# Optimization experiments

Hardware: AMD Instinct MI355X
Metric: run time of the kernel (lower is better)

The kernel has to match this reference:

```python
import jax, jax.numpy as jnp
import numpy as np

B, C, H, W = 8, 64, 256, 256
S = 512          # style_dim
K = 3            # modulated conv kernel
LRELU_SLOPE = 0.2
FUSED_SCALE = float(np.sqrt(2.0))
LIN_SCALE = 1.0 / float(np.sqrt(S))          # EqualLinear scale
CONV_SCALE = 1.0 / float(np.sqrt(C * K * K)) # ModulatedConv2d scale


def setup_inputs() -> dict:
    key = jax.random.key(0)
    ks = jax.random.split(key, 8)
    kaiming = float(np.sqrt(2.0 / (C * 9)))  # torch Conv2d default-ish init scale
    return {
        "x": jax.random.normal(ks[0], (B, C, H, W), jnp.float32),
        "style": jax.random.normal(ks[1], (B, S), jnp.float32),
        # bottleneck_IR block 1 (bn=False -> Identity norms, shortcut=identity)
        "w1a": jax.random.normal(ks[2], (C, C, 3, 3), jnp.float32) * kaiming,
        "alpha1": jnp.full((C,), 0.25, jnp.float32),
        "w1b": jax.random.normal(ks[3], (C, C, 3, 3), jnp.float32) * kaiming,
        # bottleneck_IR block 2
        "w2a": jax.random.normal(ks[4], (C, C, 3, 3), jnp.float32) * kaiming,
        "alpha2": jnp.full((C,), 0.25, jnp.float32),
        "w2b": jax.random.normal(ks[5], (C, C, 3, 3), jnp.float32) * kaiming,
        # ModulatedConv2d: EqualLinear(S->C, bias_init=1) + weight [out,in,k,k]
        "mod_w": jax.random.normal(ks[6], (C, S), jnp.float32),
        "mod_b": jnp.ones((C,), jnp.float32),
        "conv_w": jax.random.normal(ks[7], (C, C, K, K), jnp.float32),
        # FusedLeakyReLU bias
        "fused_b": jnp.zeros((C,), jnp.float32),
    }


def _conv3(x, w):
    return jax.lax.conv_general_dilated(
        x, w, (1, 1), "SAME", dimension_numbers=("NCHW", "OIHW", "NCHW"))


def _prelu(x, a):
    return jnp.where(x > 0, x, a[None, :, None, None] * x)


def _bottleneck_ir(x, wa, alpha, wb):
    # shortcut is identity (in_channel==depth, stride=1); norms are Identity (bn=False)
    return x + _conv3(_prelu(_conv3(x, wa), alpha), wb)


def reference(x, style, w1a, alpha1, w1b, w2a, alpha2, w2b,
              mod_w, mod_b, conv_w, fused_b):
    h = _bottleneck_ir(x, w1a, alpha1, w1b)
    h = _bottleneck_ir(h, w2a, alpha2, w2b)

    # ModulatedConv2d (stride 1, no up/down sample, demodulate=True)
    s = style @ (mod_w.T * LIN_SCALE) + mod_b              # [B, Cin]
    w = CONV_SCALE * conv_w[None] * s[:, None, :, None, None]  # [B, Cout, Cin, K, K]
    demod = jax.lax.rsqrt(jnp.sum(w * w, axis=(2, 3, 4)) + 1e-8)
    w = w * demod[:, :, None, None, None]

    Bn, Cin, Hh, Ww = h.shape
    out = jax.lax.conv_general_dilated(
        h.reshape(1, Bn * Cin, Hh, Ww),            # grouped-conv trick
        w.reshape(Bn * C, Cin, K, K),
        (1, 1), "SAME",
        dimension_numbers=("NCHW", "OIHW", "NCHW"),
        feature_group_count=Bn,
    ).reshape(Bn, C, Hh, Ww)

    # FusedLeakyReLU: (x + bias) -> leaky_relu(0.2) -> * sqrt(2)
    ob = out + fused_b[None, :, None, None]
    return jnp.where(ob > 0, ob, LRELU_SLOPE * ob) * FUSED_SCALE
```

## Files before the change

### kernel.cpp

```cpp
#include <hip/hip_runtime.h>
#include <hip/hip_bf16.h>
#include <math.h>

#define BB 8
#define SS 512
#define LIN_SCALE 0.044194173824159216f
#define CONV_SCALE 0.041666666666666664f
#define SQRT2 1.4142135623730951f

typedef __attribute__((ext_vector_type(8))) short short8;
typedef __attribute__((ext_vector_type(16))) float f32x16;

__device__ __forceinline__ ushort bf16h(float v) {
    unsigned u = __float_as_uint(v);
    return (ushort)((u + 0x7fffu + ((u >> 16) & 1u)) >> 16);
}
__device__ __forceinline__ void splitv(float v, ushort& h, ushort& l) {
    h = bf16h(v);
    l = bf16h(v - __uint_as_float((unsigned)h << 16));
}
__device__ __forceinline__ float b2f(ushort u) { return __uint_as_float((unsigned)u << 16); }


__global__ void zero_k(float* z) { z[threadIdx.x] = 0.f; }

__global__ __launch_bounds__(256) void tocl_k(const float* __restrict__ x,
                                              ushort* __restrict__ oCL) {
    __shared__ float tile[64][65];
    const int blk = blockIdx.x;
    const int b = blk >> 10, rem = blk & 1023;
    const int y = rem >> 2, x0 = (rem & 3) << 6;
    const int tid = threadIdx.x, lane = tid & 63, g = tid >> 6;
    const float* xb = x + ((size_t)b << 22) + (y << 8) + x0;
    #pragma unroll
    for (int i = 0; i < 16; ++i) {
        int c = i * 4 + g;
        tile[c][lane] = xb[((size_t)c << 16) + lane];
    }
    __syncthreads();
    const int cc = tid >> 6, xx = tid & 63;
    ushort hh[16], ll[16];
    #pragma unroll
    for (int t = 0; t < 16; ++t) splitv(tile[cc * 16 + t][xx], hh[t], ll[t]);
    uint w[16];
    #pragma unroll
    for (int i = 0; i < 8; ++i) {
        w[i]     = (uint)hh[2 * i] | ((uint)hh[2 * i + 1] << 16);
        w[8 + i] = (uint)ll[2 * i] | ((uint)ll[2 * i + 1] << 16);
    }
    ushort* dst = oCL + ((((size_t)(b * 4 + cc)) << 16) + (y << 8) + x0 + xx) * 32;
    *(uint4*)(dst +  0) = make_uint4(w[0], w[1], w[2], w[3]);
    *(uint4*)(dst +  8) = make_uint4(w[4], w[5], w[6], w[7]);
    *(uint4*)(dst + 16) = make_uint4(w[8], w[9], w[10], w[11]);
    *(uint4*)(dst + 24) = make_uint4(w[12], w[13], w[14], w[15]);
}

__device__ __forceinline__ int wsrc_idx(int i, int& pl) {
    int e = i & 7;
    int j = (i % 18432) >> 3;
    int cc = i / 18432;
    int F = j >> 6, u = j & 63;
    int ln_ = u >> 1, lh_ = u & 1;
    int m = F & 1; pl = (F >> 1) & 1;
    int td = F >> 2;
    int dx = td / 3, dy = td - 3 * dx;
    int co = m * 32 + ln_;
    int ci = cc * 16 + lh_ * 8 + e;
    return (co * 64 + ci) * 9 + dy * 3 + dx;
}

__global__ void packw_k(const float* __restrict__ w, ushort* __restrict__ img) {
    int i = blockIdx.x * 256 + threadIdx.x;
    if (i >= 73728) return;
    int pl; int src = wsrc_idx(i, pl);
    ushort h, l; splitv(w[src], h, l);
    img[i] = pl ? l : h;
}

__global__ void style_s_k(const float* __restrict__ style, const float* __restrict__ mod_w,
                          const float* __restrict__ mod_b, float* __restrict__ sbuf) {
    int tid = threadIdx.x;
    int b = tid >> 6, cin = tid & 63;
    float acc = 0.f;
    for (int j = 0; j < SS; ++j) acc += style[b * SS + j] * mod_w[cin * SS + j];
    sbuf[b * 64 + cin] = acc * LIN_SCALE + mod_b[cin];
}

__global__ void demod_k(const float* __restrict__ conv_w, const float* __restrict__ sbuf,
                        float* __restrict__ demod) {
    int tid = threadIdx.x;
    int b = tid >> 6, cout = tid & 63;
    float sum = 0.f;
    for (int cin = 0; cin < 64; ++cin) {
        float m = CONV_SCALE * sbuf[b * 64 + cin];
        const float* wp = conv_w + (cout * 64 + cin) * 9;
        #pragma unroll
        for (int k = 0; k < 9; ++k) { float v = wp[k] * m; sum += v * v; }
    }
    demod[b * 64 + cout] = 1.0f / sqrtf(sum + 1e-8f);
}

__global__ void packmod_k(const float* __restrict__ conv_w, const float* __restrict__ sbuf,
                          const float* __restrict__ demod, ushort* __restrict__ img) {
    int i = blockIdx.x * 256 + threadIdx.x;
    if (i >= 589824) return;
    int b = i / 73728, ii = i % 73728;
    int pl; int src = wsrc_idx(ii, pl);
    int co = src / 576; int ci = (src / 9) % 64;
    float v = CONV_SCALE * conv_w[src] * sbuf[b * 64 + ci] * demod[b * 64 + co];
    ushort h, l; splitv(v, h, l);
    img[i] = pl ? l : h;
}

#define GLDS(gsrc, ldst) __builtin_amdgcn_global_load_lds( \
    (const __attribute__((address_space(1))) unsigned int*)(gsrc), \
    (__attribute__((address_space(3))) unsigned int*)(ldst), 16, 0, 0)

#define VWAIT0 asm volatile("s_waitcnt vmcnt(0)" ::: "memory")
#define BAR    __builtin_amdgcn_s_barrier()
#define SCB    __builtin_amdgcn_sched_barrier(0)
#define MFMA32(a, bb, c) __builtin_amdgcn_mfma_f32_32x32x16_bf16(a, bb, c, 0, 0, 0)

template <int EPI, int PERB>
__global__ __launch_bounds__(256, 1)
void mconv_k(const ushort* __restrict__ inCL, const ushort* __restrict__ wimg,
             const float* __restrict__ aux, const ushort* __restrict__ rCL,
             ushort* __restrict__ oCL, float* __restrict__ onchw,
             const ushort* __restrict__ zb) {
    __shared__ __align__(16) char lds[155648];
    const int tid = threadIdx.x;
    const int orig = blockIdx.x;
    const int blk = (orig & 7) * 128 + (orig >> 3);
    const int b = blk >> 7, t7 = blk & 127;
    const int y0 = (t7 >> 3) << 4, x0 = (t7 & 7) << 5;
    const int wv = tid >> 6, l = tid & 63, ln = l & 31, lh = l >> 5;

    const ushort* wsrc = wimg + (PERB ? (size_t)b * 73728 : 0);

    f32x16 acc[2][4];
    #pragma unroll
    for (int m = 0; m < 2; ++m)
        #pragma unroll
        for (int j = 0; j < 4; ++j) acc[m][j] = (f32x16)(0.0f);

#define ISSUE_IN(cc, bo) { \
    _Pragma("unroll") for (int r_ = 0; r_ < 10; ++r_) { \
        const int s_ = r_ * 256 + tid; \
        const int p_ = s_ >> 2, sp_ = s_ & 3; \
        const int k_ = (sp_ - (p_ >> 1)) & 3; \
        const int row_ = p_ / 34, u_ = p_ - row_ * 34; \
        const int gy_ = y0 - 1 + row_, gx_ = x0 + u_ - 1; \
        const bool ok_ = ((unsigned)gy_ < 256u) & ((unsigned)gx_ < 256u) & (p_ < 612); \
        const ushort* src_ = ok_ \
            ? inCL + ((((size_t)(b * 4 + (cc))) << 16) + (gy_ << 8) + gx_) * 32 + k_ * 8 \
            : zb; \
        GLDS(src_, lds + (bo) + r_ * 4096 + (tid & 192) * 16); \
    } }

#define ISSUE_W(cc, bo) { \
    const ushort* wsB_ = wsrc + (cc) * 18432; \
    _Pragma("unroll") for (int r_ = 0; r_ < 9; ++r_) \
        GLDS(wsB_ + r_ * 2048 + tid * 8, lds + (bo) + r_ * 4096 + (tid & 192) * 16); }

#define PHASE(C, DX) { \
    const char* ib_ = lds + ((C) & 1) * 40960; \
    const char* wb_ = lds + 81920 + ((C) & 1) * 36864; \
    short8 bH_[6], bL_[6]; \
    _Pragma("unroll") for (int r_ = 0; r_ < 6; ++r_) { \
        const int p_ = (4 * wv + r_) * 34 + ln + (DX); \
        const int gH_ = 4 * p_ + ((lh + (p_ >> 1)) & 3); \
        const int gL_ = 4 * p_ + ((2 + lh + (p_ >> 1)) & 3); \
        bH_[r_] = *(const short8*)(ib_ + gH_ * 16); \
        bL_[r_] = *(const short8*)(ib_ + gL_ * 16); \
    } \
    _Pragma("unroll") for (int dy_ = 0; dy_ < 3; ++dy_) { \
        const char* wa_ = wb_ + ((DX) * 3 + dy_) * 4096 + (ln * 2 + lh) * 16; \
        const short8 aH0_ = *(const short8*)(wa_); \
        const short8 aH1_ = *(const short8*)(wa_ + 1024); \
        const short8 aL0_ = *(const short8*)(wa_ + 2048); \
        const short8 aL1_ = *(const short8*)(wa_ + 3072); \
        _Pragma("unroll") for (int j_ = 0; j_ < 4; ++j_) { \
            const int r_ = j_ + dy_; \
            acc[0][j_] = MFMA32(aH0_, bH_[r_], acc[0][j_]); \
            acc[0][j_] = MFMA32(aH0_, bL_[r_], acc[0][j_]); \
            acc[0][j_] = MFMA32(aL0_, bH_[r_], acc[0][j_]); \
            acc[1][j_] = MFMA32(aH1_, bH_[r_], acc[1][j_]); \
            acc[1][j_] = MFMA32(aH1_, bL_[r_], acc[1][j_]); \
            acc[1][j_] = MFMA32(aL1_, bH_[r_], acc[1][j_]); \
        } \
    } }

#define CHUNK(C) { \
    if ((C) < 3) { ISSUE_IN((C) + 1, (((C) + 1) & 1) * 40960); \
                   ISSUE_W((C) + 1, 81920 + (((C) + 1) & 1) * 36864); } \
    PHASE(C, 0); PHASE(C, 1); PHASE(C, 2); \
    if ((C) < 3) { SCB; VWAIT0; BAR; SCB; } }

    ISSUE_IN(0, 0);
    ISSUE_W(0, 81920);
    SCB; VWAIT0; BAR; SCB;

    CHUNK(0); CHUNK(1); CHUNK(2); CHUNK(3);

#undef ISSUE_IN
#undef ISSUE_W
#undef PHASE
#undef CHUNK

    #pragma unroll
    for (int m = 0; m < 2; ++m)
        #pragma unroll
        for (int j = 0; j < 4; ++j) {
            const int yo = y0 + 4 * wv + j;
            const int pixel = (yo << 8) + x0 + ln;
            #pragma unroll
            for (int q = 0; q < 4; ++q) {
                const int co0 = m * 32 + 8 * q + 4 * lh;
                float v0 = acc[m][j][4 * q + 0], v1 = acc[m][j][4 * q + 1];
                float v2 = acc[m][j][4 * q + 2], v3 = acc[m][j][4 * q + 3];
                const int cc_o = co0 >> 4, ch = co0 & 15;
                const size_t gbase = ((((size_t)(b * 4 + cc_o)) << 16) + pixel) * 32 + ch;
                if (EPI == 0) {
                    float4 al = *(const float4*)(aux + co0);
                    v0 = v0 > 0.f ? v0 : al.x * v0;
                    v1 = v1 > 0.f ? v1 : al.y * v1;
                    v2 = v2 > 0.f ? v2 : al.z * v2;
                    v3 = v3 > 0.f ? v3 : al.w * v3;
                } else if (EPI == 1) {
                    ushort4 rh = *(const ushort4*)(rCL + gbase);
                    ushort4 rl = *(const ushort4*)(rCL + gbase + 16);
                    v0 += b2f(rh.x) + b2f(rl.x);
                    v1 += b2f(rh.y) + b2f(rl.y);
                    v2 += b2f(rh.z) + b2f(rl.z);
                    v3 += b2f(rh.w) + b2f(rl.w);
                } else {
                    float4 bi = *(const float4*)(aux + co0);
                    float ob;
                    ob = v0 + bi.x; v0 = (ob > 0.f ? ob : 0.2f * ob) * SQRT2;
                    ob = v1 + bi.y; v1 = (ob > 0.f ? ob : 0.2f * ob) * SQRT2;
                    ob = v2 + bi.z; v2 = (ob > 0.f ? ob : 0.2f * ob) * SQRT2;
                    ob = v3 + bi.w; v3 = (ob > 0.f ? ob : 0.2f * ob) * SQRT2;
                }
                if (EPI == 2) {
                    const size_t sp = (size_t)pixel;
                    onchw[(((size_t)(b * 64 + co0 + 0)) << 16) + sp] = v0;
                    onchw[(((size_t)(b * 64 + co0 + 1)) << 16) + sp] = v1;
                    onchw[(((size_t)(b * 64 + co0 + 2)) << 16) + sp] = v2;
                    onchw[(((size_t)(b * 64 + co0 + 3)) << 16) + sp] = v3;
                } else {
                    ushort4 h4, l4;
                    splitv(v0, h4.x, l4.x); splitv(v1, h4.y, l4.y);
                    splitv(v2, h4.z, l4.z); splitv(v3, h4.w, l4.w);
                    *(ushort4*)(oCL + gbase) = h4;
                    *(ushort4*)(oCL + gbase + 16) = l4;
                }
            }
        }
}

extern "C" void kernel_launch(void* const* d_in, const int* in_sizes, int n_in,
                              void* d_out, int out_size, void* d_ws, size_t ws_size,
                              hipStream_t stream) {
    const float* x       = (const float*)d_in[0];
    const float* style   = (const float*)d_in[1];
    const float* w1a     = (const float*)d_in[2];
    const float* alpha1  = (const float*)d_in[3];
    const float* w1b     = (const float*)d_in[4];
    const float* w2a     = (const float*)d_in[5];
    const float* alpha2  = (const float*)d_in[6];
    const float* w2b     = (const float*)d_in[7];
    const float* mod_w   = (const float*)d_in[8];
    const float* mod_b   = (const float*)d_in[9];
    const float* conv_w  = (const float*)d_in[10];
    const float* fused_b = (const float*)d_in[11];
    float* out = (float*)d_out;

    char* ws = (char*)d_ws;
    float*  zbf   = (float*)ws;
    float*  sbuf  = (float*)(ws + 256);
    float*  demod = (float*)(ws + 2304);
    ushort* wfix  = (ushort*)(ws + 4352);
    ushort* wmod  = (ushort*)(ws + 594176);
    char*   pl    = ws + 1774080;
    const size_t PAIRB = 134217728ull;

    ushort* XP = (ushort*)pl;
    ushort* PB = (ushort*)(pl + PAIRB);
    ushort* PA;
    if (ws_size >= 1774080ull + 3 * PAIRB) PA = (ushort*)(pl + 2 * PAIRB);
    else                                   PA = (ushort*)d_out;
    const ushort* zb = (const ushort*)zbf;

    hipLaunchKernelGGL(zero_k, dim3(1), dim3(64), 0, stream, zbf);
    hipLaunchKernelGGL(tocl_k, dim3(BB * 1024), dim3(256), 0, stream, x, XP);
    hipLaunchKernelGGL(packw_k, dim3(288), dim3(256), 0, stream, w1a, wfix + 0 * 73728);
    hipLaunchKernelGGL(packw_k, dim3(288), dim3(256), 0, stream, w1b, wfix + 1 * 73728);
    hipLaunchKernelGGL(packw_k, dim3(288), dim3(256), 0, stream, w2a, wfix + 2 * 73728);
    hipLaunchKernelGGL(packw_k, dim3(288), dim3(256), 0, stream, w2b, wfix + 3 * 73728);
    hipLaunchKernelGGL(style_s_k, dim3(1), dim3(512), 0, stream, style, mod_w, mod_b, sbuf);
    hipLaunchKernelGGL(demod_k, dim3(1), dim3(512), 0, stream, conv_w, sbuf, demod);
    hipLaunchKernelGGL(packmod_k, dim3(2304), dim3(256), 0, stream, conv_w, sbuf, demod, wmod);

    const dim3 cgrid(1024), cblk(256);
    hipLaunchKernelGGL((mconv_k<0, 0>), cgrid, cblk, 0, stream,
        XP, wfix + 0 * 73728, alpha1, (const ushort*)nullptr, PA, (float*)nullptr, zb);
    hipLaunchKernelGGL((mconv_k<1, 0>), cgrid, cblk, 0, stream,
        PA, wfix + 1 * 73728, (const float*)nullptr, XP, PB, (float*)nullptr, zb);
    hipLaunchKernelGGL((mconv_k<0, 0>), cgrid, cblk, 0, stream,
        PB, wfix + 2 * 73728, alpha2, (const ushort*)nullptr, PA, (float*)nullptr, zb);
    hipLaunchKernelGGL((mconv_k<1, 0>), cgrid, cblk, 0, stream,
        PA, wfix + 3 * 73728, (const float*)nullptr, PB, PB, (float*)nullptr, zb);
    hipLaunchKernelGGL((mconv_k<2, 1>), cgrid, cblk, 0, stream,
        PB, wmod, fused_b, (const ushort*)nullptr, (ushort*)nullptr, out, zb);
}
```

Before: 964.0 us.

## Halve conv tile height, stream weights from global into registers, double occupancy

Changes the conv tile from 16x32 to 8x32 pixels, which doubles the grid, and cuts LDS to about 43KB so two blocks can share a CU (launch bounds set to 2). Weight fragments are no longer staged through LDS. Each lane now loads them from global memory into double-buffered registers, and the weight image layout is repacked so lane-contiguous reads work. It also adds s_setprio around the MFMA bursts and a partial vmcnt wait that lets in-flight register weight loads overlap the barrier. The cost is more redundant halo loads per output pixel, higher register pressure, and relying on global/L2 latency for the weight fetches.

```diff
diff --git a/kernel.cpp b/kernel.cpp
--- a/kernel.cpp
+++ b/kernel.cpp
@@ -55,25 +55,24 @@
     *(uint4*)(dst + 24) = make_uint4(w[12], w[13], w[14], w[15]);
 }
 
-__device__ __forceinline__ int wsrc_idx(int i, int& pl) {
-    int e = i & 7;
-    int j = (i % 18432) >> 3;
-    int cc = i / 18432;
-    int F = j >> 6, u = j & 63;
-    int ln_ = u >> 1, lh_ = u & 1;
-    int m = F & 1; pl = (F >> 1) & 1;
-    int td = F >> 2;
-    int dx = td / 3, dy = td - 3 * dx;
-    int co = m * 32 + ln_;
-    int ci = cc * 16 + lh_ * 8 + e;
-    return (co * 64 + ci) * 9 + dy * 3 + dx;
+__device__ __forceinline__ void wdecode(int i, int& c, int& tap, int& co, int& ci, int& pl) {
+    int e = i & 7;  int t = i >> 3;
+    int lh = t & 1; t >>= 1;
+    co = t & 63;    t >>= 6;
+    pl = t & 1;     t >>= 1;
+    int dy = t % 3; t /= 3;
+    int dx = t % 3; t /= 3;
+    c = t;
+    ci = c * 16 + lh * 8 + e;
+    tap = dy * 3 + dx;
 }
 
 __global__ void packw_k(const float* __restrict__ w, ushort* __restrict__ img) {
     int i = blockIdx.x * 256 + threadIdx.x;
     if (i >= 73728) return;
-    int pl; int src = wsrc_idx(i, pl);
-    ushort h, l; splitv(w[src], h, l);
+    int c, tap, co, ci, pl;
+    wdecode(i, c, tap, co, ci, pl);
+    ushort h, l; splitv(w[(co * 64 + ci) * 9 + tap], h, l);
     img[i] = pl ? l : h;
 }
 
@@ -105,9 +104,9 @@
     int i = blockIdx.x * 256 + threadIdx.x;
     if (i >= 589824) return;
     int b = i / 73728, ii = i % 73728;
-    int pl; int src = wsrc_idx(ii, pl);
-    int co = src / 576; int ci = (src / 9) % 64;
-    float v = CONV_SCALE * conv_w[src] * sbuf[b * 64 + ci] * demod[b * 64 + co];
+    int c, tap, co, ci, pl;
+    wdecode(ii, c, tap, co, ci, pl);
+    float v = CONV_SCALE * conv_w[(co * 64 + ci) * 9 + tap] * sbuf[b * 64 + ci] * demod[b * 64 + co];
     ushort h, l; splitv(v, h, l);
     img[i] = pl ? l : h;
 }
@@ -116,102 +115,121 @@
     (const __attribute__((address_space(1))) unsigned int*)(gsrc), \
     (__attribute__((address_space(3))) unsigned int*)(ldst), 16, 0, 0)
 
-#define VWAIT0 asm volatile("s_waitcnt vmcnt(0)" ::: "memory")
-#define BAR    __builtin_amdgcn_s_barrier()
-#define SCB    __builtin_amdgcn_sched_barrier(0)
+#define VWAIT12 asm volatile("s_waitcnt vmcnt(12)" ::: "memory")
+#define BAR     __builtin_amdgcn_s_barrier()
+#define SCB     __builtin_amdgcn_sched_barrier(0)
 #define MFMA32(a, bb, c) __builtin_amdgcn_mfma_f32_32x32x16_bf16(a, bb, c, 0, 0, 0)
 
 template <int EPI, int PERB>
-__global__ __launch_bounds__(256, 1)
+__global__ __launch_bounds__(256, 2)
 void mconv_k(const ushort* __restrict__ inCL, const ushort* __restrict__ wimg,
              const float* __restrict__ aux, const ushort* __restrict__ rCL,
              ushort* __restrict__ oCL, float* __restrict__ onchw,
              const ushort* __restrict__ zb) {
-    __shared__ __align__(16) char lds[155648];
+    __shared__ __align__(16) char lds[43520];
     const int tid = threadIdx.x;
     const int orig = blockIdx.x;
-    const int blk = (orig & 7) * 128 + (orig >> 3);
-    const int b = blk >> 7, t7 = blk & 127;
-    const int y0 = (t7 >> 3) << 4, x0 = (t7 & 7) << 5;
+    const int blk = (orig & 7) * 256 + (orig >> 3);
+    const int b = blk >> 8, t8 = blk & 255;
+    const int y0 = (t8 >> 3) << 3, x0 = (t8 & 7) << 5;
     const int wv = tid >> 6, l = tid & 63, ln = l & 31, lh = l >> 5;
 
     const ushort* wsrc = wimg + (PERB ? (size_t)b * 73728 : 0);
-
-    f32x16 acc[2][4];
+    const int aoff = ln * 16 + lh * 8;
+
+    f32x16 acc[2][2];
     #pragma unroll
     for (int m = 0; m < 2; ++m)
         #pragma unroll
-        for (int j = 0; j < 4; ++j) acc[m][j] = (f32x16)(0.0f);
+        for (int j = 0; j < 2; ++j) acc[m][j] = (f32x16)(0.0f);
+
+    short8 A0H[3][2], A0L[3][2], A1H[3][2], A1L[3][2];
 
 #define ISSUE_IN(cc, bo) { \
-    _Pragma("unroll") for (int r_ = 0; r_ < 10; ++r_) { \
-        const int s_ = r_ * 256 + tid; \
-        const int p_ = s_ >> 2, sp_ = s_ & 3; \
+    _Pragma("unroll") for (int r_ = 0; r_ < 5; ++r_) { \
+        const int G_ = r_ * 256 + tid; \
+        const int p_ = G_ >> 2, sp_ = G_ & 3; \
         const int k_ = (sp_ - (p_ >> 1)) & 3; \
         const int row_ = p_ / 34, u_ = p_ - row_ * 34; \
         const int gy_ = y0 - 1 + row_, gx_ = x0 + u_ - 1; \
-        const bool ok_ = ((unsigned)gy_ < 256u) & ((unsigned)gx_ < 256u) & (p_ < 612); \
+        const bool ok_ = ((unsigned)gy_ < 256u) & ((unsigned)gx_ < 256u); \
         const ushort* src_ = ok_ \
             ? inCL + ((((size_t)(b * 4 + (cc))) << 16) + (gy_ << 8) + gx_) * 32 + k_ * 8 \
             : zb; \
         GLDS(src_, lds + (bo) + r_ * 4096 + (tid & 192) * 16); \
+    } \
+    { const int G_ = 1280 + tid; \
+      const int p_ = G_ >> 2, sp_ = G_ & 3; \
+      const int k_ = (sp_ - (p_ >> 1)) & 3; \
+      const int row_ = p_ / 34, u_ = p_ - row_ * 34; \
+      const int gy_ = y0 - 1 + row_, gx_ = x0 + u_ - 1; \
+      const bool ok_ = (tid < 80) & ((unsigned)gy_ < 256u) & ((unsigned)gx_ < 256u); \
+      const ushort* src_ = ok_ \
+          ? inCL + ((((size_t)(b * 4 + (cc))) << 16) + (gy_ << 8) + gx_) * 32 + k_ * 8 \
+          : zb; \
+      if (tid < 80) GLDS(src_, lds + (bo) + 20480 + (tid & 192) * 16); } }
+
+#define LOADA(BNK, C, DX) { \
+    _Pragma("unroll") for (int dy_ = 0; dy_ < 3; ++dy_) { \
+        const ushort* ab_ = wsrc + (size_t)(((C) * 3 + (DX)) * 3 + dy_) * 2048 + aoff; \
+        BNK##H[dy_][0] = *(const short8*)ab_; \
+        BNK##H[dy_][1] = *(const short8*)(ab_ + 512); \
+        BNK##L[dy_][0] = *(const short8*)(ab_ + 1024); \
+        BNK##L[dy_][1] = *(const short8*)(ab_ + 1536); \
     } }
 
-#define ISSUE_W(cc, bo) { \
-    const ushort* wsB_ = wsrc + (cc) * 18432; \
-    _Pragma("unroll") for (int r_ = 0; r_ < 9; ++r_) \
-        GLDS(wsB_ + r_ * 2048 + tid * 8, lds + (bo) + r_ * 4096 + (tid & 192) * 16); }
-
-#define PHASE(C, DX) { \
-    const char* ib_ = lds + ((C) & 1) * 40960; \
-    const char* wb_ = lds + 81920 + ((C) & 1) * 36864; \
-    short8 bH_[6], bL_[6]; \
-    _Pragma("unroll") for (int r_ = 0; r_ < 6; ++r_) { \
-        const int p_ = (4 * wv + r_) * 34 + ln + (DX); \
+#define PHASE(C, DX, CUR) { \
+    const char* ib_ = lds + ((C) & 1) * 21760; \
+    short8 bH_[4], bL_[4]; \
+    _Pragma("unroll") for (int r_ = 0; r_ < 4; ++r_) { \
+        const int p_ = (2 * wv + r_) * 34 + ln + (DX); \
         const int gH_ = 4 * p_ + ((lh + (p_ >> 1)) & 3); \
         const int gL_ = 4 * p_ + ((2 + lh + (p_ >> 1)) & 3); \
         bH_[r_] = *(const short8*)(ib_ + gH_ * 16); \
         bL_[r_] = *(const short8*)(ib_ + gL_ * 16); \
     } \
-    _Pragma("unroll") for (int dy_ = 0; dy_ < 3; ++dy_) { \
-        const char* wa_ = wb_ + ((DX) * 3 + dy_) * 4096 + (ln * 2 + lh) * 16; \
-        const short8 aH0_ = *(const short8*)(wa_); \
-        const short8 aH1_ = *(const short8*)(wa_ + 1024); \
-        const short8 aL0_ = *(const short8*)(wa_ + 2048); \
-        const short8 aL1_ = *(const short8*)(wa_ + 3072); \
-        _Pragma("unroll") for (int j_ = 0; j_ < 4; ++j_) { \
+    __builtin_amdgcn_s_setprio(1); \
+    _Pragma("unroll") for (int dy_ = 0; dy_ < 3; ++dy_) \
+        _Pragma("unroll") for (int j_ = 0; j_ < 2; ++j_) { \
             const int r_ = j_ + dy_; \
-            acc[0][j_] = MFMA32(aH0_, bH_[r_], acc[0][j_]); \
-            acc[0][j_] = MFMA32(aH0_, bL_[r_], acc[0][j_]); \
-            acc[0][j_] = MFMA32(aL0_, bH_[r_], acc[0][j_]); \
-            acc[1][j_] = MFMA32(aH1_, bH_[r_], acc[1][j_]); \
-            acc[1][j_] = MFMA32(aH1_, bL_[r_], acc[1][j_]); \
-            acc[1][j_] = MFMA32(aL1_, bH_[r_], acc[1][j_]); \
+            acc[0][j_] = MFMA32(CUR##H[dy_][0], bH_[r_], acc[0][j_]); \
+            acc[0][j_] = MFMA32(CUR##H[dy_][0], bL_[r_], acc[0][j_]); \
+            acc[0][j_] = MFMA32(CUR##L[dy_][0], bH_[r_], acc[0][j_]); \
+            acc[1][j_] = MFMA32(CUR##H[dy_][1], bH_[r_], acc[1][j_]); \
+            acc[1][j_] = MFMA32(CUR##H[dy_][1], bL_[r_], acc[1][j_]); \
+            acc[1][j_] = MFMA32(CUR##L[dy_][1], bH_[r_], acc[1][j_]); \
         } \
-    } }
-
-#define CHUNK(C) { \
-    if ((C) < 3) { ISSUE_IN((C) + 1, (((C) + 1) & 1) * 40960); \
-                   ISSUE_W((C) + 1, 81920 + (((C) + 1) & 1) * 36864); } \
-    PHASE(C, 0); PHASE(C, 1); PHASE(C, 2); \
-    if ((C) < 3) { SCB; VWAIT0; BAR; SCB; } }
+    __builtin_amdgcn_s_setprio(0); }
 
     ISSUE_IN(0, 0);
-    ISSUE_W(0, 81920);
-    SCB; VWAIT0; BAR; SCB;
-
-    CHUNK(0); CHUNK(1); CHUNK(2); CHUNK(3);
+    LOADA(A0, 0, 0);
+    SCB; VWAIT12; BAR; SCB;
+
+    ISSUE_IN(1, 21760); LOADA(A1, 0, 1); PHASE(0, 0, A0);
+    LOADA(A0, 0, 2);                     PHASE(0, 1, A1);
+    LOADA(A1, 1, 0);                     PHASE(0, 2, A0);
+    SCB; VWAIT12; BAR; SCB;
+    ISSUE_IN(2, 0);     LOADA(A0, 1, 1); PHASE(1, 0, A1);
+    LOADA(A1, 1, 2);                     PHASE(1, 1, A0);
+    LOADA(A0, 2, 0);                     PHASE(1, 2, A1);
+    SCB; VWAIT12; BAR; SCB;
+    ISSUE_IN(3, 21760); LOADA(A1, 2, 1); PHASE(2, 0, A0);
+    LOADA(A0, 2, 2);                     PHASE(2, 1, A1);
+    LOADA(A1, 3, 0);                     PHASE(2, 2, A0);
+    SCB; VWAIT12; BAR; SCB;
+    LOADA(A0, 3, 1); PHASE(3, 0, A1);
+    LOADA(A1, 3, 2); PHASE(3, 1, A0);
+    PHASE(3, 2, A1);
 
 #undef ISSUE_IN
-#undef ISSUE_W
+#undef LOADA
 #undef PHASE
-#undef CHUNK
 
     #pragma unroll
     for (int m = 0; m < 2; ++m)
         #pragma unroll
-        for (int j = 0; j < 4; ++j) {
-            const int yo = y0 + 4 * wv + j;
+        for (int j = 0; j < 2; ++j) {
+            const int yo = y0 + 2 * wv + j;
             const int pixel = (yo << 8) + x0 + ln;
             #pragma unroll
             for (int q = 0; q < 4; ++q) {
@@ -301,7 +319,7 @@
     hipLaunchKernelGGL(demod_k, dim3(1), dim3(512), 0, stream, conv_w, sbuf, demod);
     hipLaunchKernelGGL(packmod_k, dim3(2304), dim3(256), 0, stream, conv_w, sbuf, demod, wmod);
 
-    const dim3 cgrid(1024), cblk(256);
+    const dim3 cgrid(2048), cblk(256);
     hipLaunchKernelGGL((mconv_k<0, 0>), cgrid, cblk, 0, stream,
         XP, wfix + 0 * 73728, alpha1, (const ushort*)nullptr, PA, (float*)nullptr, zb);
     hipLaunchKernelGGL((mconv_k<1, 0>), cgrid, cblk, 0, stream,
```

Result: no change. 951.0 us (-1.3%).

## Load input tiles directly to registers, shrink LDS for two blocks per CU

Applied to the files above, without the earlier changes.

Input activation tiles are no longer staged through LDS. Each lane now loads its high and low bf16 halves straight from global memory into registers, prefetching the next phase's high part while the current phase computes. LDS holds only the double-buffered weights, so it shrinks enough for launch bounds of two blocks per CU. MFMA sections are wrapped in raised wave priority, and the wait relaxes to vmcnt(6). The risks are redundant global loads across overlapping 3x3 halos, higher register pressure under the two-block bound, and a correctness dependence on the vmcnt counting matching the issued loads.

```diff
diff --git a/kernel.cpp b/kernel.cpp
--- a/kernel.cpp
+++ b/kernel.cpp
@@ -116,18 +116,18 @@
     (const __attribute__((address_space(1))) unsigned int*)(gsrc), \
     (__attribute__((address_space(3))) unsigned int*)(ldst), 16, 0, 0)
 
-#define VWAIT0 asm volatile("s_waitcnt vmcnt(0)" ::: "memory")
+#define VWAIT6 asm volatile("s_waitcnt vmcnt(6)" ::: "memory")
 #define BAR    __builtin_amdgcn_s_barrier()
 #define SCB    __builtin_amdgcn_sched_barrier(0)
 #define MFMA32(a, bb, c) __builtin_amdgcn_mfma_f32_32x32x16_bf16(a, bb, c, 0, 0, 0)
 
 template <int EPI, int PERB>
-__global__ __launch_bounds__(256, 1)
+__global__ __launch_bounds__(256, 2)
 void mconv_k(const ushort* __restrict__ inCL, const ushort* __restrict__ wimg,
              const float* __restrict__ aux, const ushort* __restrict__ rCL,
              ushort* __restrict__ oCL, float* __restrict__ onchw,
              const ushort* __restrict__ zb) {
-    __shared__ __align__(16) char lds[155648];
+    __shared__ __align__(16) char lds[73728];
     const int tid = threadIdx.x;
     const int orig = blockIdx.x;
     const int blk = (orig & 7) * 128 + (orig >> 3);
@@ -136,6 +136,8 @@
     const int wv = tid >> 6, l = tid & 63, ln = l & 31, lh = l >> 5;
 
     const ushort* wsrc = wimg + (PERB ? (size_t)b * 73728 : 0);
+    const int gx = x0 + ln - 1;
+    const size_t breg = (size_t)(b * 4) << 16;
 
     f32x16 acc[2][4];
     #pragma unroll
@@ -143,69 +145,75 @@
         #pragma unroll
         for (int j = 0; j < 4; ++j) acc[m][j] = (f32x16)(0.0f);
 
-#define ISSUE_IN(cc, bo) { \
-    _Pragma("unroll") for (int r_ = 0; r_ < 10; ++r_) { \
-        const int s_ = r_ * 256 + tid; \
-        const int p_ = s_ >> 2, sp_ = s_ & 3; \
-        const int k_ = (sp_ - (p_ >> 1)) & 3; \
-        const int row_ = p_ / 34, u_ = p_ - row_ * 34; \
-        const int gy_ = y0 - 1 + row_, gx_ = x0 + u_ - 1; \
-        const bool ok_ = ((unsigned)gy_ < 256u) & ((unsigned)gx_ < 256u) & (p_ < 612); \
-        const ushort* src_ = ok_ \
-            ? inCL + ((((size_t)(b * 4 + (cc))) << 16) + (gy_ << 8) + gx_) * 32 + k_ * 8 \
-            : zb; \
-        GLDS(src_, lds + (bo) + r_ * 4096 + (tid & 192) * 16); \
-    } }
+    short8 B0[6], B1[6];
 
 #define ISSUE_W(cc, bo) { \
     const ushort* wsB_ = wsrc + (cc) * 18432; \
     _Pragma("unroll") for (int r_ = 0; r_ < 9; ++r_) \
         GLDS(wsB_ + r_ * 2048 + tid * 8, lds + (bo) + r_ * 4096 + (tid & 192) * 16); }
 
-#define PHASE(C, DX) { \
-    const char* ib_ = lds + ((C) & 1) * 40960; \
-    const char* wb_ = lds + 81920 + ((C) & 1) * 36864; \
-    short8 bH_[6], bL_[6]; \
+#define PRE_H(BNK, CC, DX) { \
     _Pragma("unroll") for (int r_ = 0; r_ < 6; ++r_) { \
-        const int p_ = (4 * wv + r_) * 34 + ln + (DX); \
-        const int gH_ = 4 * p_ + ((lh + (p_ >> 1)) & 3); \
-        const int gL_ = 4 * p_ + ((2 + lh + (p_ >> 1)) & 3); \
-        bH_[r_] = *(const short8*)(ib_ + gH_ * 16); \
-        bL_[r_] = *(const short8*)(ib_ + gL_ * 16); \
-    } \
+        const int gy_ = y0 + 4 * wv - 1 + r_; \
+        const int gxx_ = gx + (DX); \
+        const bool ok_ = ((unsigned)gy_ < 256u) & ((unsigned)gxx_ < 256u); \
+        const ushort* a_ = ok_ \
+            ? inCL + ((breg + ((size_t)(CC) << 16) + (gy_ << 8) + gxx_) * 32 + lh * 8) \
+            : zb; \
+        BNK[r_] = *(const short8*)a_; \
+    } }
+
+#define LOAD_L(DST, CC, DX) { \
+    _Pragma("unroll") for (int r_ = 0; r_ < 6; ++r_) { \
+        const int gy_ = y0 + 4 * wv - 1 + r_; \
+        const int gxx_ = gx + (DX); \
+        const bool ok_ = ((unsigned)gy_ < 256u) & ((unsigned)gxx_ < 256u); \
+        const ushort* a_ = ok_ \
+            ? inCL + ((breg + ((size_t)(CC) << 16) + (gy_ << 8) + gxx_) * 32 + 16 + lh * 8) \
+            : zb; \
+        DST[r_] = *(const short8*)a_; \
+    } }
+
+#define PH(p, CUR, NXT) { \
+    const int C_ = (p) / 3, DX_ = (p) % 3; \
+    if ((p) < 11) PRE_H(NXT, ((p) + 1) / 3, ((p) + 1) % 3); \
+    short8 bl_[6]; \
+    LOAD_L(bl_, C_, DX_); \
+    const char* wb_ = lds + (C_ & 1) * 36864; \
+    __builtin_amdgcn_s_setprio(1); \
     _Pragma("unroll") for (int dy_ = 0; dy_ < 3; ++dy_) { \
-        const char* wa_ = wb_ + ((DX) * 3 + dy_) * 4096 + (ln * 2 + lh) * 16; \
+        const char* wa_ = wb_ + (DX_ * 3 + dy_) * 4096 + (ln * 2 + lh) * 16; \
         const short8 aH0_ = *(const short8*)(wa_); \
         const short8 aH1_ = *(const short8*)(wa_ + 1024); \
         const short8 aL0_ = *(const short8*)(wa_ + 2048); \
         const short8 aL1_ = *(const short8*)(wa_ + 3072); \
         _Pragma("unroll") for (int j_ = 0; j_ < 4; ++j_) { \
             const int r_ = j_ + dy_; \
-            acc[0][j_] = MFMA32(aH0_, bH_[r_], acc[0][j_]); \
-            acc[0][j_] = MFMA32(aH0_, bL_[r_], acc[0][j_]); \
-            acc[0][j_] = MFMA32(aL0_, bH_[r_], acc[0][j_]); \
-            acc[1][j_] = MFMA32(aH1_, bH_[r_], acc[1][j_]); \
-            acc[1][j_] = MFMA32(aH1_, bL_[r_], acc[1][j_]); \
-            acc[1][j_] = MFMA32(aL1_, bH_[r_], acc[1][j_]); \
+            acc[0][j_] = MFMA32(aH0_, CUR[r_], acc[0][j_]); \
+            acc[0][j_] = MFMA32(aH0_, bl_[r_], acc[0][j_]); \
+            acc[0][j_] = MFMA32(aL0_, CUR[r_], acc[0][j_]); \
+            acc[1][j_] = MFMA32(aH1_, CUR[r_], acc[1][j_]); \
+            acc[1][j_] = MFMA32(aH1_, bl_[r_], acc[1][j_]); \
+            acc[1][j_] = MFMA32(aL1_, CUR[r_], acc[1][j_]); \
         } \
-    } }
-
-#define CHUNK(C) { \
-    if ((C) < 3) { ISSUE_IN((C) + 1, (((C) + 1) & 1) * 40960); \
-                   ISSUE_W((C) + 1, 81920 + (((C) + 1) & 1) * 36864); } \
-    PHASE(C, 0); PHASE(C, 1); PHASE(C, 2); \
-    if ((C) < 3) { SCB; VWAIT0; BAR; SCB; } }
-
-    ISSUE_IN(0, 0);
-    ISSUE_W(0, 81920);
-    SCB; VWAIT0; BAR; SCB;
-
-    CHUNK(0); CHUNK(1); CHUNK(2); CHUNK(3);
-
-#undef ISSUE_IN
+    } \
+    __builtin_amdgcn_s_setprio(0); \
+    if (DX_ == 0 && C_ < 3) { ISSUE_W(C_ + 1, ((C_ + 1) & 1) * 36864); } \
+    if (DX_ == 2 && (p) < 11) { SCB; VWAIT6; BAR; SCB; } }
+
+    ISSUE_W(0, 0);
+    PRE_H(B0, 0, 0);
+    SCB; VWAIT6; BAR; SCB;
+
+    PH(0, B0, B1);  PH(1, B1, B0);  PH(2, B0, B1);
+    PH(3, B1, B0);  PH(4, B0, B1);  PH(5, B1, B0);
+    PH(6, B0, B1);  PH(7, B1, B0);  PH(8, B0, B1);
+    PH(9, B1, B0);  PH(10, B0, B1); PH(11, B1, B0);
+
 #undef ISSUE_W
-#undef PHASE
-#undef CHUNK
+#undef PRE_H
+#undef LOAD_L
+#undef PH
 
     #pragma unroll
     for (int m = 0; m < 2; ++m)
```

Result: faster. 922.8 us (-4.3%).
